# Optimization experiments

Hardware: AMD Instinct MI355X
Metric: run time of the kernel (lower is better)

Reference implementation:

```python
import jax, jax.numpy as jnp
import numpy as np

B, S, C, H, EPS = 8, 1024, 768, 12, 1e-6
D = C // H            # head dim 64
F_HID = int(C * 4.0)  # 3072


def _layer_norm(x, w, b):
    mu = jnp.mean(x, axis=-1, keepdims=True)
    var = jnp.mean(jnp.square(x - mu), axis=-1, keepdims=True)
    return (x - mu) * jax.lax.rsqrt(var + EPS) * w + b


def setup_inputs() -> dict:
    key = jax.random.key(0)
    ks = jax.random.split(key, 16)
    sc_c = 1.0 / np.sqrt(C)
    sc_f = 1.0 / np.sqrt(F_HID)
    return {
        "hidden_states": jax.random.normal(ks[0], (B, S, C), jnp.float32),
        "ln1_w": jnp.ones((C,), jnp.float32),
        "ln1_b": jnp.zeros((C,), jnp.float32),
        # weights stored [in, out] (transpose of torch Linear layout; same math)
        "q_w": jax.random.normal(ks[1], (C, C), jnp.float32) * sc_c,
        "q_b": jnp.zeros((C,), jnp.float32),
        "k_w": jax.random.normal(ks[2], (C, C), jnp.float32) * sc_c,
        "k_b": jnp.zeros((C,), jnp.float32),
        "v_w": jax.random.normal(ks[3], (C, C), jnp.float32) * sc_c,
        "v_b": jnp.zeros((C,), jnp.float32),
        "o_w": jax.random.normal(ks[4], (C, C), jnp.float32) * sc_c,
        "o_b": jnp.zeros((C,), jnp.float32),
        "lam1": jnp.ones((C,), jnp.float32),
        "ln2_w": jnp.ones((C,), jnp.float32),
        "ln2_b": jnp.zeros((C,), jnp.float32),
        "fc1_w": jax.random.normal(ks[5], (C, F_HID), jnp.float32) * sc_c,
        "fc1_b": jnp.zeros((F_HID,), jnp.float32),
        "fc2_w": jax.random.normal(ks[6], (F_HID, C), jnp.float32) * sc_f,
        "fc2_b": jnp.zeros((C,), jnp.float32),
    }


def reference(hidden_states, ln1_w, ln1_b, q_w, q_b, k_w, k_b, v_w, v_b,
              o_w, o_b, lam1, ln2_w, ln2_b, fc1_w, fc1_b, fc2_w, fc2_b):
    shortcut = hidden_states
    x = _layer_norm(hidden_states, ln1_w, ln1_b)
    # QKV projections, split heads: [B,S,C] -> [B,H,S,D]
    def heads(t):
        return t.reshape(B, S, H, D).transpose(0, 2, 1, 3)
    q = heads(x @ q_w + q_b)
    k = heads(x @ k_w + k_b)
    v = heads(x @ v_w + v_b)
    scores = jnp.einsum("bhsd,bhtd->bhst", q, k) / np.sqrt(D)
    probs = jax.nn.softmax(scores, axis=-1)  # dropout p=0 -> identity
    ctx = jnp.einsum("bhst,bhtd->bhsd", probs, v)
    ctx = ctx.transpose(0, 2, 1, 3).reshape(B, S, C)
    attn_out = ctx @ o_w + o_b
    hidden = attn_out * lam1 + shortcut
    y = _layer_norm(hidden, ln2_w, ln2_b)
    y = jax.nn.gelu(y @ fc1_w + fc1_b, approximate=False)
    y = y @ fc2_w + fc2_b
    return y * lam2_mul(lam1) + hidden if False else (y * jnp.ones_like(lam1) * lam1 * 0 + y) * 0 + y * lam1 * 0 + (y * _LAM2 + hidden)


# NOTE: layer_scale2 has its own parameter; expose it cleanly instead of the hack above.
_LAM2 = None

def lam2_mul(x):
    return x

# Clean final definitions (override the above):

def setup_inputs() -> dict:  # noqa: F811
    key = jax.random.key(0)
    ks = jax.random.split(key, 16)
    sc_c = 1.0 / np.sqrt(C)
    sc_f = 1.0 / np.sqrt(F_HID)
    return {
        "hidden_states": jax.random.normal(ks[0], (B, S, C), jnp.float32),
        "ln1_w": jnp.ones((C,), jnp.float32),
        "ln1_b": jnp.zeros((C,), jnp.float32),
        "q_w": jax.random.normal(ks[1], (C, C), jnp.float32) * sc_c,
        "q_b": jnp.zeros((C,), jnp.float32),
        "k_w": jax.random.normal(ks[2], (C, C), jnp.float32) * sc_c,
        "k_b": jnp.zeros((C,), jnp.float32),
        "v_w": jax.random.normal(ks[3], (C, C), jnp.float32) * sc_c,
        "v_b": jnp.zeros((C,), jnp.float32),
        "o_w": jax.random.normal(ks[4], (C, C), jnp.float32) * sc_c,
        "o_b": jnp.zeros((C,), jnp.float32),
        "lam1": jnp.ones((C,), jnp.float32),
        "ln2_w": jnp.ones((C,), jnp.float32),
        "ln2_b": jnp.zeros((C,), jnp.float32),
        "fc1_w": jax.random.normal(ks[5], (C, F_HID), jnp.float32) * sc_c,
        "fc1_b": jnp.zeros((F_HID,), jnp.float32),
        "fc2_w": jax.random.normal(ks[6], (F_HID, C), jnp.float32) * sc_f,
        "fc2_b": jnp.zeros((C,), jnp.float32),
        "lam2": jnp.ones((C,), jnp.float32),
    }


def reference(hidden_states, ln1_w, ln1_b, q_w, q_b, k_w, k_b, v_w, v_b,  # noqa: F811
              o_w, o_b, lam1, ln2_w, ln2_b, fc1_w, fc1_b, fc2_w, fc2_b, lam2):
    shortcut = hidden_states
    x = _layer_norm(hidden_states, ln1_w, ln1_b)
    def heads(t):
        return t.reshape(B, S, H, D).transpose(0, 2, 1, 3)  # [B,H,S,D]
    q = heads(x @ q_w + q_b)
    k = heads(x @ k_w + k_b)
    v = heads(x @ v_w + v_b)
    scores = jnp.einsum("bhsd,bhtd->bhst", q, k) / np.sqrt(D)
    probs = jax.nn.softmax(scores, axis=-1)  # attn dropout p=0 (eval)
    ctx = jnp.einsum("bhst,bhtd->bhsd", probs, v)
    ctx = ctx.transpose(0, 2, 1, 3).reshape(B, S, C)
    attn_out = ctx @ o_w + o_b            # SelfOutput dense (dropout p=0)
    hidden = attn_out * lam1 + shortcut   # layer_scale1 + residual
    y = _layer_norm(hidden, ln2_w, ln2_b)
    y = jax.nn.gelu(y @ fc1_w + fc1_b, approximate=False)  # nn.GELU exact
    y = y @ fc2_w + fc2_b
    return y * lam2 + hidden              # layer_scale2 + residual
```

## Files before the change

kernel.cpp:

```cpp
#include <hip/hip_runtime.h>
#include <hip/hip_bf16.h>
#include <stdint.h>
#include <stddef.h>

using bf16x8 = __attribute__((ext_vector_type(8))) short;
using f32x4  = __attribute__((ext_vector_type(4))) float;
using f32x16 = __attribute__((ext_vector_type(16))) float;

#define DEV static __device__ __forceinline__

DEV unsigned short f2bf(float f) {
  union { float f; uint32_t u; } x; x.f = f;
  uint32_t u = x.u;
  u += 0x7fffu + ((u >> 16) & 1u);
  return (unsigned short)(u >> 16);
}

DEV uint32_t pkbf(float a, float b) {
  __hip_bfloat162 t = __float22bfloat162_rn(float2{a, b});
  union { __hip_bfloat162 h; uint32_t u; } c; c.h = t; return c.u;
}

DEV void gld_lds16(const void* g, void* lds) {
  __builtin_amdgcn_global_load_lds(
      (__attribute__((address_space(1))) void*)(uintptr_t)g,
      (__attribute__((address_space(3))) void*)(uintptr_t)lds, 16, 0, 0);
}

__global__ void transpose_w(const float* __restrict__ in, unsigned short* __restrict__ out,
                            int K, int N) {
  __shared__ float tile[64][65];
  int n0 = blockIdx.x * 64, k0 = blockIdx.y * 64;
  int tx = threadIdx.x & 15, ty = threadIdx.x >> 4;
#pragma unroll
  for (int j = 0; j < 4; ++j) {
    int r = ty + j * 16;
    float4 v = *(const float4*)(in + (size_t)(k0 + r) * N + n0 + tx * 4);
    tile[r][tx * 4 + 0] = v.x; tile[r][tx * 4 + 1] = v.y;
    tile[r][tx * 4 + 2] = v.z; tile[r][tx * 4 + 3] = v.w;
  }
  __syncthreads();
#pragma unroll
  for (int j = 0; j < 4; ++j) {
    int n = ty + j * 16;
    ushort4 o;
    o.x = f2bf(tile[tx * 4 + 0][n]);
    o.y = f2bf(tile[tx * 4 + 1][n]);
    o.z = f2bf(tile[tx * 4 + 2][n]);
    o.w = f2bf(tile[tx * 4 + 3][n]);
    *(ushort4*)(out + (size_t)(n0 + n) * K + k0 + tx * 4) = o;
  }
}

__global__ void transpose_v(const unsigned short* __restrict__ v,
                            unsigned short* __restrict__ vt) {
  __shared__ unsigned short tile[64][72];
  const int bh = blockIdx.y;
  const int s0 = blockIdx.x * 64;
  const unsigned short* src = v  + (size_t)bh * 1024 * 64;
  unsigned short* dst       = vt + (size_t)bh * 64 * 1024;
  const int tid = threadIdx.x;
#pragma unroll
  for (int j = 0; j < 2; ++j) {
    int idx = tid + j * 256;
    int s = idx >> 3, c = (idx & 7) * 8;
    *(uint4*)&tile[s][c] = *(const uint4*)(src + (size_t)(s0 + s) * 64 + c);
  }
  __syncthreads();
#pragma unroll
  for (int j = 0; j < 2; ++j) {
    int idx = tid + j * 256;
    int d = idx >> 3, sc = (idx & 7) * 8;
    uint32_t t0 = (uint32_t)tile[sc + 0][d] | ((uint32_t)tile[sc + 1][d] << 16);
    uint32_t t1 = (uint32_t)tile[sc + 2][d] | ((uint32_t)tile[sc + 3][d] << 16);
    uint32_t t2 = (uint32_t)tile[sc + 4][d] | ((uint32_t)tile[sc + 5][d] << 16);
    uint32_t t3 = (uint32_t)tile[sc + 6][d] | ((uint32_t)tile[sc + 7][d] << 16);
    uint4 o; o.x = t0; o.y = t1; o.z = t2; o.w = t3;
    *(uint4*)(dst + (size_t)d * 1024 + s0 + sc) = o;
  }
}

__global__ void pack_bias(const float* __restrict__ q, const float* __restrict__ k,
                          const float* __restrict__ v, float* __restrict__ out) {
  int i = blockIdx.x * 256 + threadIdx.x;
  const float* s = (i < 768) ? q : ((i < 1536) ? k : v);
  int r = i; if (r >= 1536) r -= 1536; else if (r >= 768) r -= 768;
  out[i] = s[r];
}

__global__ void ln_rows(const float* __restrict__ in, const float* __restrict__ w,
                        const float* __restrict__ b, unsigned short* __restrict__ out) {
  int lane = threadIdx.x & 63;
  int row = blockIdx.x * 4 + (threadIdx.x >> 6);
  const float* p = in + (size_t)row * 768;
  float4 v[3];
  float s = 0.f, s2 = 0.f;
#pragma unroll
  for (int j = 0; j < 3; ++j) {
    v[j] = *(const float4*)(p + j * 256 + lane * 4);
    s  += v[j].x + v[j].y + v[j].z + v[j].w;
    s2 += v[j].x * v[j].x + v[j].y * v[j].y + v[j].z * v[j].z + v[j].w * v[j].w;
  }
#pragma unroll
  for (int o = 32; o >= 1; o >>= 1) { s += __shfl_xor(s, o); s2 += __shfl_xor(s2, o); }
  float mu = s * (1.f / 768.f);
  float var = s2 * (1.f / 768.f) - mu * mu;
  float rs = rsqrtf(var + 1e-6f);
#pragma unroll
  for (int j = 0; j < 3; ++j) {
    int c = j * 256 + lane * 4;
    float4 wv = *(const float4*)(w + c);
    float4 bv = *(const float4*)(b + c);
    ushort4 o4;
    o4.x = f2bf((v[j].x - mu) * rs * wv.x + bv.x);
    o4.y = f2bf((v[j].y - mu) * rs * wv.y + bv.y);
    o4.z = f2bf((v[j].z - mu) * rs * wv.z + bv.z);
    o4.w = f2bf((v[j].w - mu) * rs * wv.w + bv.w);
    *(ushort4*)(out + (size_t)row * 768 + c) = o4;
  }
}

template <int EP>
__global__ void gemm_bf16(const unsigned short* __restrict__ A,
                          const unsigned short* __restrict__ BT,
                          const float* __restrict__ bias,
                          int N, int K,
                          void* __restrict__ out,
                          const float* __restrict__ scale,
                          const float* __restrict__ addv,
                          unsigned short* __restrict__ q_out,
                          unsigned short* __restrict__ k_out,
                          unsigned short* __restrict__ v_out) {
  __shared__ unsigned short As[3][128 * 32];
  __shared__ unsigned short Bs[3][128 * 32];
  const int wid = threadIdx.x >> 6, lane = threadIdx.x & 63;
  const int bm = blockIdx.y * 128, bn = blockIdx.x * 128;
  const int wr = wid >> 1, wc = wid & 1;
  const int NT = K >> 5;

  auto stage = [&](int t, int buf) {
    int k0 = t << 5;
#pragma unroll
    for (int j = 0; j < 2; ++j) {
      int seg = wid * 2 + j;
      int row = seg * 16 + (lane >> 2);
      int kc = k0 + (lane & 3) * 8;
      gld_lds16(A  + (size_t)(bm + row) * K + kc, (char*)As[buf] + seg * 1024);
      gld_lds16(BT + (size_t)(bn + row) * K + kc, (char*)Bs[buf] + seg * 1024);
    }
  };

  f32x4 acc[4][4] = {};

  stage(0, 0);
  if (NT > 1) {
    stage(1, 1);
    asm volatile("s_waitcnt vmcnt(4)" ::: "memory");
  } else {
    asm volatile("s_waitcnt vmcnt(0)" ::: "memory");
  }
  __builtin_amdgcn_sched_barrier(0);
  __builtin_amdgcn_s_barrier();
  __builtin_amdgcn_sched_barrier(0);

  for (int t = 0; t < NT; ++t) {
    if (t + 2 < NT) stage(t + 2, (t + 2) % 3);
    const unsigned short* Ab = As[t % 3];
    const unsigned short* Bb = Bs[t % 3];
    bf16x8 af[4], bfr[4];
#pragma unroll
    for (int i = 0; i < 4; ++i)
      af[i] = *(const bf16x8*)(Ab + (wr * 64 + i * 16 + (lane & 15)) * 32 + (lane >> 4) * 8);
#pragma unroll
    for (int i = 0; i < 4; ++i)
      bfr[i] = *(const bf16x8*)(Bb + (wc * 64 + i * 16 + (lane & 15)) * 32 + (lane >> 4) * 8);
#pragma unroll
    for (int mi = 0; mi < 4; ++mi)
#pragma unroll
      for (int ni = 0; ni < 4; ++ni)
        acc[mi][ni] = __builtin_amdgcn_mfma_f32_16x16x32_bf16(af[mi], bfr[ni], acc[mi][ni], 0, 0, 0);
    if (t + 2 < NT)      { asm volatile("s_waitcnt vmcnt(4)" ::: "memory"); }
    else if (t + 1 < NT) { asm volatile("s_waitcnt vmcnt(0)" ::: "memory"); }
    __builtin_amdgcn_sched_barrier(0);
    __builtin_amdgcn_s_barrier();
    __builtin_amdgcn_sched_barrier(0);
  }

#pragma unroll
  for (int mi = 0; mi < 4; ++mi) {
#pragma unroll
    for (int ni = 0; ni < 4; ++ni) {
      int col = bn + wc * 64 + ni * 16 + (lane & 15);
      float bcol = bias[col];
#pragma unroll
      for (int r = 0; r < 4; ++r) {
        int row = bm + wr * 64 + mi * 16 + (lane >> 4) * 4 + r;
        float v = acc[mi][ni][r] + bcol;
        if (EP == 0) {
          int b = row >> 10, s = row & 1023;
          int piece = col / 768;
          int rc = col - piece * 768;
          int h = rc >> 6, d = rc & 63;
          unsigned short bvv = f2bf(v);
          size_t idx = ((size_t)(b * 12 + h) * 1024 + s) * 64 + d;
          if (piece == 0)      q_out[idx] = bvv;
          else if (piece == 1) k_out[idx] = bvv;
          else                 v_out[idx] = bvv;
        } else if (EP == 1) {
          ((float*)out)[(size_t)row * 768 + col] = v * scale[col] + addv[(size_t)row * 768 + col];
        } else if (EP == 2) {
          float g = 0.5f * v * (1.f + erff(v * 0.70710678118654752f));
          ((unsigned short*)out)[(size_t)row * (size_t)N + col] = f2bf(g);
        } else {
          ((float*)out)[(size_t)row * 768 + col] = v * scale[col] + addv[(size_t)row * 768 + col];
        }
      }
    }
  }
}

__global__ __launch_bounds__(256) void attn_fwd(const unsigned short* __restrict__ qb,
                         const unsigned short* __restrict__ kb,
                         const unsigned short* __restrict__ vtb,
                         unsigned short* __restrict__ ctx) {
  __shared__ unsigned short Ks[2][64 * 64];
  __shared__ unsigned short VTs[2][64 * 64];
  __shared__ float alphaW[4][32];
  const int tid = threadIdx.x;
  const int wid = tid >> 6, lane = tid & 63;
  const int l31 = lane & 31;
  const bool hi = lane >= 32;
  const int hi8 = hi ? 8 : 0, hi16 = hi ? 16 : 0;
  const int sw0 = (l31 & 7) << 4;
  const int wg = (blockIdx.x & 7) * 96 + (blockIdx.x >> 3);
  const int bh = wg >> 3, qt = wg & 7;
  const int b = bh / 12, h = bh % 12;
  const unsigned short* qh  = qb  + (size_t)bh * 1024 * 64;
  const unsigned short* kh  = kb  + (size_t)bh * 1024 * 64;
  const unsigned short* vth = vtb + (size_t)bh * 64 * 1024;

  const int qrow = qt * 128 + wid * 32 + l31;
  bf16x8 qf[4];
#pragma unroll
  for (int kf = 0; kf < 4; ++kf)
    qf[kf] = *(const bf16x8*)(qh + (size_t)qrow * 64 + kf * 16 + hi8);

  bf16x8 ones;
#pragma unroll
  for (int i = 0; i < 8; ++i) ones[i] = (short)0x3F80;

  f32x16 o0 = {}, o1 = {}, l_acc = {};
  float mcol = -1e30f;
  const float sc = 0.125f * 1.44269504088896f;

  const int r1 = tid >> 3;
  const int sl = tid & 7;
  const int cb = (sl * 16) ^ ((r1 & 7) << 4);

  {
    uint4 k0v = *(const uint4*)(kh + (size_t)r1 * 64 + sl * 8);
    uint4 k1v = *(const uint4*)(kh + (size_t)(r1 + 32) * 64 + sl * 8);
    uint4 v0v = *(const uint4*)(vth + (size_t)r1 * 1024 + sl * 8);
    uint4 v1v = *(const uint4*)(vth + (size_t)(r1 + 32) * 1024 + sl * 8);
    *(uint4*)((char*)Ks[0]  + r1 * 128 + cb) = k0v;
    *(uint4*)((char*)Ks[0]  + (r1 + 32) * 128 + cb) = k1v;
    *(uint4*)((char*)VTs[0] + r1 * 128 + cb) = v0v;
    *(uint4*)((char*)VTs[0] + (r1 + 32) * 128 + cb) = v1v;
  }

  uint4 kA, kB, vA, vB;
  for (int t = 0; t < 16; ++t) {
    if (t < 15) {
      const int s1 = (t + 1) * 64;
      kA = *(const uint4*)(kh + (size_t)(s1 + r1) * 64 + sl * 8);
      kB = *(const uint4*)(kh + (size_t)(s1 + r1 + 32) * 64 + sl * 8);
      vA = *(const uint4*)(vth + (size_t)r1 * 1024 + s1 + sl * 8);
      vB = *(const uint4*)(vth + (size_t)(r1 + 32) * 1024 + s1 + sl * 8);
    }
    asm volatile("s_waitcnt lgkmcnt(0)" ::: "memory");
    __builtin_amdgcn_s_barrier();
    const char* KsB  = (const char*)Ks[t & 1];
    const char* VTsB = (const char*)VTs[t & 1];

    f32x16 s0 = {}, s1v = {};
#pragma unroll
    for (int kf = 0; kf < 4; ++kf) {
      bf16x8 k0 = *(const bf16x8*)(KsB + l31 * 128 + ((kf * 32 + hi16) ^ sw0));
      bf16x8 k1 = *(const bf16x8*)(KsB + (l31 + 32) * 128 + ((kf * 32 + hi16) ^ sw0));
      s0  = __builtin_amdgcn_mfma_f32_32x32x16_bf16(k0, qf[kf], s0, 0, 0, 0);
      s1v = __builtin_amdgcn_mfma_f32_32x32x16_bf16(k1, qf[kf], s1v, 0, 0, 0);
    }

    float mt = s0[0];
#pragma unroll
    for (int i = 1; i < 16; ++i) mt = fmaxf(mt, s0[i]);
#pragma unroll
    for (int i = 0; i < 16; ++i) mt = fmaxf(mt, s1v[i]);
    mt *= sc;
    mt = fmaxf(mt, __shfl_xor(mt, 32));

    if (__ballot(mt > mcol + 8.f)) {
      float mnew = fmaxf(mcol, mt);
      float a = exp2f(mcol - mnew);
      if (lane < 32) alphaW[wid][lane] = a;
      mcol = mnew;
      asm volatile("s_waitcnt lgkmcnt(0)" ::: "memory");
      __builtin_amdgcn_sched_barrier(0);
#pragma unroll
      for (int r = 0; r < 16; ++r) {
        float av = alphaW[wid][(r & 3) + ((r >> 2) << 3) + (hi ? 4 : 0)];
        o0[r] *= av; o1[r] *= av; l_acc[r] *= av;
      }
    }

    float p0[16], p1[16];
#pragma unroll
    for (int i = 0; i < 16; ++i) p0[i] = exp2f(s0[i] * sc - mcol);
#pragma unroll
    for (int i = 0; i < 16; ++i) p1[i] = exp2f(s1v[i] * sc - mcol);
    uint32_t W[16], X[16];
#pragma unroll
    for (int i = 0; i < 8; ++i) {
      W[i]     = pkbf(p0[2 * i], p0[2 * i + 1]);
      W[8 + i] = pkbf(p1[2 * i], p1[2 * i + 1]);
    }
#pragma unroll
    for (int i = 0; i < 16; ++i) X[i] = (uint32_t)__shfl_xor((int)W[i], 32);
    bf16x8 pa[4];
    {
      union U4 { uint32_t u[4]; bf16x8 v; } f;
      f.u[0] = hi ? X[2] : W[0];  f.u[1] = hi ? X[3] : W[1];
      f.u[2] = hi ? W[2] : X[0];  f.u[3] = hi ? W[3] : X[1];   pa[0] = f.v;
      f.u[0] = hi ? X[6] : W[4];  f.u[1] = hi ? X[7] : W[5];
      f.u[2] = hi ? W[6] : X[4];  f.u[3] = hi ? W[7] : X[5];   pa[1] = f.v;
      f.u[0] = hi ? X[10] : W[8]; f.u[1] = hi ? X[11] : W[9];
      f.u[2] = hi ? W[10] : X[8]; f.u[3] = hi ? W[11] : X[9];  pa[2] = f.v;
      f.u[0] = hi ? X[14] : W[12]; f.u[1] = hi ? X[15] : W[13];
      f.u[2] = hi ? W[14] : X[12]; f.u[3] = hi ? W[15] : X[13]; pa[3] = f.v;
    }

#pragma unroll
    for (int f = 0; f < 4; ++f) {
      l_acc = __builtin_amdgcn_mfma_f32_32x32x16_bf16(pa[f], ones, l_acc, 0, 0, 0);
      bf16x8 v0 = *(const bf16x8*)(VTsB + l31 * 128 + ((f * 32 + hi16) ^ sw0));
      bf16x8 v1 = *(const bf16x8*)(VTsB + (l31 + 32) * 128 + ((f * 32 + hi16) ^ sw0));
      o0 = __builtin_amdgcn_mfma_f32_32x32x16_bf16(pa[f], v0, o0, 0, 0, 0);
      o1 = __builtin_amdgcn_mfma_f32_32x32x16_bf16(pa[f], v1, o1, 0, 0, 0);
    }

    if (t < 15) {
      asm volatile("s_waitcnt vmcnt(0)" ::: "memory");
      __builtin_amdgcn_sched_barrier(0);
      char* Kn = (char*)Ks[(t + 1) & 1];
      char* Vn = (char*)VTs[(t + 1) & 1];
      *(uint4*)(Kn + r1 * 128 + cb) = kA;
      *(uint4*)(Kn + (r1 + 32) * 128 + cb) = kB;
      *(uint4*)(Vn + r1 * 128 + cb) = vA;
      *(uint4*)(Vn + (r1 + 32) * 128 + cb) = vB;
    }
  }

#pragma unroll
  for (int r = 0; r < 16; ++r) {
    int rq = (r & 3) + ((r >> 2) << 3) + (hi ? 4 : 0);
    int srow = qt * 128 + wid * 32 + rq;
    float inv = 1.f / l_acc[r];
    size_t base = ((size_t)(b * 1024 + srow)) * 768 + h * 64;
    ctx[base + l31]      = f2bf(o0[r] * inv);
    ctx[base + 32 + l31] = f2bf(o1[r] * inv);
  }
}

extern "C" void kernel_launch(void* const* d_in, const int* in_sizes, int n_in,
                              void* d_out, int out_size, void* d_ws, size_t ws_size,
                              hipStream_t stream) {
  const float* hs    = (const float*)d_in[0];
  const float* ln1_w = (const float*)d_in[1];
  const float* ln1_b = (const float*)d_in[2];
  const float* q_w   = (const float*)d_in[3];
  const float* q_b   = (const float*)d_in[4];
  const float* k_w   = (const float*)d_in[5];
  const float* k_b   = (const float*)d_in[6];
  const float* v_w   = (const float*)d_in[7];
  const float* v_b   = (const float*)d_in[8];
  const float* o_w   = (const float*)d_in[9];
  const float* o_b   = (const float*)d_in[10];
  const float* lam1  = (const float*)d_in[11];
  const float* ln2_w = (const float*)d_in[12];
  const float* ln2_b = (const float*)d_in[13];
  const float* fc1_w = (const float*)d_in[14];
  const float* fc1_b = (const float*)d_in[15];
  const float* fc2_w = (const float*)d_in[16];
  const float* fc2_b = (const float*)d_in[17];
  const float* lam2  = (const float*)d_in[18];

  char* ws = (char*)d_ws;
  size_t off = 0;
  auto carve = [&](size_t bytes) { char* p = ws + off; off += (bytes + 255) & ~(size_t)255; return p; };
  unsigned short* wqkv_t = (unsigned short*)carve((size_t)2304 * 768 * 2);
  unsigned short* wo_t   = (unsigned short*)carve((size_t)768 * 768 * 2);
  unsigned short* wfc1_t = (unsigned short*)carve((size_t)3072 * 768 * 2);
  unsigned short* wfc2_t = (unsigned short*)carve((size_t)768 * 3072 * 2);
  float*          bqkv   = (float*)carve(2304 * 4);
  const size_t SB = (size_t)8192 * 768 * 2;
  char* unionA = carve(4 * SB);
  unsigned short* x_ln   = (unsigned short*)unionA;
  unsigned short* q_buf  = (unsigned short*)(unionA + SB);
  unsigned short* k_buf  = (unsigned short*)(unionA + 2 * SB);
  unsigned short* vt_buf = (unsigned short*)(unionA + 3 * SB);
  unsigned short* act    = (unsigned short*)unionA;
  unsigned short* ctx    = (unsigned short*)carve(SB);
  float*          hidden2= (float*)carve((size_t)8192 * 768 * 4);
  unsigned short* y_ln   = (unsigned short*)carve(SB);
  unsigned short* v_buf  = (unsigned short*)hidden2;

  pack_bias<<<dim3(9), dim3(256), 0, stream>>>(q_b, k_b, v_b, bqkv);
  transpose_w<<<dim3(12, 12), dim3(256), 0, stream>>>(q_w, wqkv_t, 768, 768);
  transpose_w<<<dim3(12, 12), dim3(256), 0, stream>>>(k_w, wqkv_t + (size_t)768 * 768, 768, 768);
  transpose_w<<<dim3(12, 12), dim3(256), 0, stream>>>(v_w, wqkv_t + (size_t)2 * 768 * 768, 768, 768);
  transpose_w<<<dim3(12, 12), dim3(256), 0, stream>>>(o_w, wo_t, 768, 768);
  transpose_w<<<dim3(48, 12), dim3(256), 0, stream>>>(fc1_w, wfc1_t, 768, 3072);
  transpose_w<<<dim3(12, 48), dim3(256), 0, stream>>>(fc2_w, wfc2_t, 3072, 768);

  ln_rows<<<dim3(2048), dim3(256), 0, stream>>>(hs, ln1_w, ln1_b, x_ln);
  gemm_bf16<0><<<dim3(18, 64), dim3(256), 0, stream>>>(x_ln, wqkv_t, bqkv, 2304, 768,
      nullptr, nullptr, nullptr, q_buf, k_buf, v_buf);
  transpose_v<<<dim3(16, 96), dim3(256), 0, stream>>>(v_buf, vt_buf);
  attn_fwd<<<dim3(768), dim3(256), 0, stream>>>(q_buf, k_buf, vt_buf, ctx);
  gemm_bf16<1><<<dim3(6, 64), dim3(256), 0, stream>>>(ctx, wo_t, o_b, 768, 768,
      hidden2, lam1, hs, nullptr, nullptr, nullptr);
  ln_rows<<<dim3(2048), dim3(256), 0, stream>>>(hidden2, ln2_w, ln2_b, y_ln);
  gemm_bf16<2><<<dim3(24, 64), dim3(256), 0, stream>>>(y_ln, wfc1_t, fc1_b, 3072, 768,
      act, nullptr, nullptr, nullptr, nullptr, nullptr);
  gemm_bf16<3><<<dim3(6, 64), dim3(256), 0, stream>>>(act, wfc2_t, fc2_b, 768, 3072,
      d_out, lam2, hidden2, nullptr, nullptr, nullptr);
}
```

Before: 414.5 us.

## Swizzle GEMM LDS tiles and merge weight preprocessing into one launch

Applies an XOR swizzle to the 16-byte k-chunks written into shared memory by the GEMM loads and matches it in the fragment reads, to reduce LDS bank conflicts. Also folds the bias packing and six weight transpose launches into one preprocess kernel, cutting launch overhead. The swizzle relies on the staging and read index mappings staying consistent.

```diff
diff --git a/kernel.cpp b/kernel.cpp
--- a/kernel.cpp
+++ b/kernel.cpp
@@ -27,11 +27,36 @@
       (__attribute__((address_space(3))) void*)(uintptr_t)lds, 16, 0, 0);
 }
 
-__global__ void transpose_w(const float* __restrict__ in, unsigned short* __restrict__ out,
-                            int K, int N) {
+__global__ void preprocess(const float* __restrict__ q_w, const float* __restrict__ k_w,
+                           const float* __restrict__ v_w, const float* __restrict__ o_w,
+                           const float* __restrict__ fc1_w, const float* __restrict__ fc2_w,
+                           const float* __restrict__ q_b, const float* __restrict__ k_b,
+                           const float* __restrict__ v_b,
+                           unsigned short* __restrict__ wqkv_t, unsigned short* __restrict__ wo_t,
+                           unsigned short* __restrict__ wfc1_t, unsigned short* __restrict__ wfc2_t,
+                           float* __restrict__ bqkv) {
+  const int blk = blockIdx.x;
+  if (blk >= 1728) {
+    int i = (blk - 1728) * 256 + threadIdx.x;
+    const float* s = (i < 768) ? q_b : ((i < 1536) ? k_b : v_b);
+    int r = i; if (r >= 1536) r -= 1536; else if (r >= 768) r -= 768;
+    bqkv[i] = s[r];
+    return;
+  }
+  const float* in; unsigned short* out; int K, N, nx, local;
+  if (blk < 576) {
+    local = blk % 144; int wsel = blk / 144;
+    K = 768; N = 768; nx = 12;
+    in  = (wsel == 0) ? q_w : (wsel == 1) ? k_w : (wsel == 2) ? v_w : o_w;
+    out = (wsel < 3) ? (wqkv_t + (size_t)wsel * 768 * 768) : wo_t;
+  } else if (blk < 1152) {
+    local = blk - 576; K = 768; N = 3072; nx = 48; in = fc1_w; out = wfc1_t;
+  } else {
+    local = blk - 1152; K = 3072; N = 768; nx = 12; in = fc2_w; out = wfc2_t;
+  }
+  const int n0 = (local % nx) * 64, k0 = (local / nx) * 64;
   __shared__ float tile[64][65];
-  int n0 = blockIdx.x * 64, k0 = blockIdx.y * 64;
-  int tx = threadIdx.x & 15, ty = threadIdx.x >> 4;
+  const int tx = threadIdx.x & 15, ty = threadIdx.x >> 4;
 #pragma unroll
   for (int j = 0; j < 4; ++j) {
     int r = ty + j * 16;
@@ -78,14 +103,6 @@
     uint4 o; o.x = t0; o.y = t1; o.z = t2; o.w = t3;
     *(uint4*)(dst + (size_t)d * 1024 + s0 + sc) = o;
   }
-}
-
-__global__ void pack_bias(const float* __restrict__ q, const float* __restrict__ k,
-                          const float* __restrict__ v, float* __restrict__ out) {
-  int i = blockIdx.x * 256 + threadIdx.x;
-  const float* s = (i < 768) ? q : ((i < 1536) ? k : v);
-  int r = i; if (r >= 1536) r -= 1536; else if (r >= 768) r -= 768;
-  out[i] = s[r];
 }
 
 __global__ void ln_rows(const float* __restrict__ in, const float* __restrict__ w,
@@ -138,17 +155,20 @@
   const int wr = wid >> 1, wc = wid & 1;
   const int NT = K >> 5;
 
+  const int kcs = 8 * ((lane & 3) ^ ((lane >> 2) & 3));
+
   auto stage = [&](int t, int buf) {
     int k0 = t << 5;
 #pragma unroll
     for (int j = 0; j < 2; ++j) {
       int seg = wid * 2 + j;
       int row = seg * 16 + (lane >> 2);
-      int kc = k0 + (lane & 3) * 8;
-      gld_lds16(A  + (size_t)(bm + row) * K + kc, (char*)As[buf] + seg * 1024);
-      gld_lds16(BT + (size_t)(bn + row) * K + kc, (char*)Bs[buf] + seg * 1024);
+      gld_lds16(A  + (size_t)(bm + row) * K + k0 + kcs, (char*)As[buf] + seg * 1024);
+      gld_lds16(BT + (size_t)(bn + row) * K + k0 + kcs, (char*)Bs[buf] + seg * 1024);
     }
   };
+
+  const int fcol = 8 * ((lane >> 4) ^ (lane & 3));
 
   f32x4 acc[4][4] = {};
 
@@ -170,10 +190,10 @@
     bf16x8 af[4], bfr[4];
 #pragma unroll
     for (int i = 0; i < 4; ++i)
-      af[i] = *(const bf16x8*)(Ab + (wr * 64 + i * 16 + (lane & 15)) * 32 + (lane >> 4) * 8);
+      af[i] = *(const bf16x8*)(Ab + (wr * 64 + i * 16 + (lane & 15)) * 32 + fcol);
 #pragma unroll
     for (int i = 0; i < 4; ++i)
-      bfr[i] = *(const bf16x8*)(Bb + (wc * 64 + i * 16 + (lane & 15)) * 32 + (lane >> 4) * 8);
+      bfr[i] = *(const bf16x8*)(Bb + (wc * 64 + i * 16 + (lane & 15)) * 32 + fcol);
 #pragma unroll
     for (int mi = 0; mi < 4; ++mi)
 #pragma unroll
@@ -414,13 +434,8 @@
   unsigned short* y_ln   = (unsigned short*)carve(SB);
   unsigned short* v_buf  = (unsigned short*)hidden2;
 
-  pack_bias<<<dim3(9), dim3(256), 0, stream>>>(q_b, k_b, v_b, bqkv);
-  transpose_w<<<dim3(12, 12), dim3(256), 0, stream>>>(q_w, wqkv_t, 768, 768);
-  transpose_w<<<dim3(12, 12), dim3(256), 0, stream>>>(k_w, wqkv_t + (size_t)768 * 768, 768, 768);
-  transpose_w<<<dim3(12, 12), dim3(256), 0, stream>>>(v_w, wqkv_t + (size_t)2 * 768 * 768, 768, 768);
-  transpose_w<<<dim3(12, 12), dim3(256), 0, stream>>>(o_w, wo_t, 768, 768);
-  transpose_w<<<dim3(48, 12), dim3(256), 0, stream>>>(fc1_w, wfc1_t, 768, 3072);
-  transpose_w<<<dim3(12, 48), dim3(256), 0, stream>>>(fc2_w, wfc2_t, 3072, 768);
+  preprocess<<<dim3(1737), dim3(256), 0, stream>>>(q_w, k_w, v_w, o_w, fc1_w, fc2_w,
+      q_b, k_b, v_b, wqkv_t, wo_t, wfc1_t, wfc2_t, bqkv);
 
   ln_rows<<<dim3(2048), dim3(256), 0, stream>>>(hs, ln1_w, ln1_b, x_ln);
   gemm_bf16<0><<<dim3(18, 64), dim3(256), 0, stream>>>(x_ln, wqkv_t, bqkv, 2304, 768,
```

New measurement: 405.8 us. -2.1%, faster.
